# Optimization experiments

Measured on AMD Instinct MI355X. Metric: run time of the kernel, lower is better.

Reference implementation:

```python
import jax, jax.numpy as jnp
import numpy as np

F_NODE, F_BOND, D, LAYERS = 133, 14, 256, 3
N_NODE, N_BOND, N_NB = 100000, 200000, 600000


def hardswish(x):
    return x * jnp.clip(x + 3.0, 0.0, 6.0) * (1.0 / 6.0)


def setup_inputs() -> dict:
    key = jax.random.key(0)
    ks = jax.random.split(key, 16)

    def xav(k, fan_in, fan_out):
        std = (2.0 / (fan_in + fan_out)) ** 0.5
        return (jax.random.normal(k, (fan_in, fan_out), jnp.float32) * std)

    inp = {
        "node": jax.random.normal(ks[0], (N_NODE, F_NODE), jnp.float32),
        "bond": jax.random.normal(ks[1], (N_BOND, F_BOND), jnp.float32),
        "connect": jax.random.randint(ks[2], (3, N_BOND), 0, N_NODE, jnp.int32),
        "bond_neighbour": jax.random.randint(ks[3], (2, N_NB), 0, N_BOND, jnp.int32),
        # learned parameters, stored as [in, out] (torch Linear transposed)
        "w_node": xav(ks[4], F_NODE, D), "b_node": jnp.zeros((D,), jnp.float32),
        "w_node_final": xav(ks[5], F_NODE + D, D), "b_node_final": jnp.zeros((D,), jnp.float32),
        "w_bond": xav(ks[6], F_NODE + F_BOND, D), "b_bond": jnp.zeros((D,), jnp.float32),
        "w_bond_final": xav(ks[7], F_NODE + F_BOND + D, D), "b_bond_final": jnp.zeros((D,), jnp.float32),
        "w_z": xav(ks[8], F_NODE + F_BOND + D, D), "b_z": jnp.zeros((D,), jnp.float32),
        "w_r": xav(ks[9], F_NODE + F_BOND + D, D), "b_r": jnp.zeros((D,), jnp.float32),
        "u": xav(ks[10], D, D),
        "w_m": xav(ks[11], F_NODE + F_BOND, D), "b_m": jnp.zeros((D,), jnp.float32),
        "w_n": xav(ks[12], F_NODE, D), "b_n": jnp.zeros((D,), jnp.float32),
        "u_n": xav(ks[13], 2 * D, D),
    }
    return inp


def reference(node, bond, connect, bond_neighbour,
              w_node, b_node, w_node_final, b_node_final,
              w_bond, b_bond, w_bond_final, b_bond_final,
              w_z, b_z, w_r, b_r, u, w_m, b_m, w_n, b_n, u_n):
    i_idx, j_idx = connect[0], connect[1]          # [E]; connect[2] (reverse) unused
    ij_idx, ki_idx = bond_neighbour[0], bond_neighbour[1]  # [E_nb]

    init_bond = jnp.concatenate([node[i_idx], bond], axis=-1)  # [E, f_node+f_bond]
    init_node = node                                           # [N, f_node]

    mess_bond = hardswish(init_bond @ w_bond + b_bond)  # [E, D]
    mess_node = hardswish(node @ w_node + b_node)       # [N, D]

    for _ in range(LAYERS):
        mess_ki = mess_bond[ki_idx]                                   # [E_nb, D]
        s_ij = jax.ops.segment_sum(mess_ki, ij_idx, num_segments=N_BOND)
        z_ij = jax.nn.sigmoid(jnp.concatenate([init_bond, s_ij], -1) @ w_z + b_z)
        r_ki = jax.nn.sigmoid(jnp.concatenate([init_bond[ij_idx], mess_ki], -1) @ w_r + b_r)
        r_ij = jax.ops.segment_sum(r_ki * mess_ki, ij_idx, num_segments=N_BOND)
        m_ij = jnp.tanh(init_bond @ w_m + b_m + r_ij @ u)
        mess_bond = (1.0 - z_ij) * s_ij + z_ij * m_ij                 # [E, D]
        aggr_node = jax.ops.segment_sum(mess_bond, j_idx, num_segments=N_NODE)
        mess_node = hardswish(init_node @ w_n + b_n
                              + jnp.concatenate([mess_node, aggr_node], -1) @ u_n)

    mess_bond = hardswish(jnp.concatenate([init_bond, mess_bond], -1) @ w_bond_final + b_bond_final)
    mess_node = hardswish(jnp.concatenate([init_node, mess_node], -1) @ w_node_final + b_node_final)
    # dropout is identity in eval mode
    return mess_node, mess_bond
```

## Files before the change

kernel.cpp:

```cpp
#include <hip/hip_runtime.h>
#include <hip/hip_bf16.h>

#define NN 100000
#define NE 200000
#define NB 600000
#define FN 133
#define FB 14
#define FIB 147
#define DD 256

typedef __hip_bfloat16 bf16;
typedef __attribute__((ext_vector_type(8))) short short8;
typedef __attribute__((ext_vector_type(4))) float f32x4;

__device__ __forceinline__ float hswish(float x) {
    float c = fminf(fmaxf(x + 3.f, 0.f), 6.f);
    return x * c * (1.f / 6.f);
}
__device__ __forceinline__ float sigmoidf(float x) {
    return 1.f / (1.f + __expf(-x));
}
__device__ __forceinline__ float tanh_fast(float x) {
    return 1.f - 2.f / (1.f + __expf(2.f * x));
}
__device__ __forceinline__ float bf2f(unsigned short u) {
    union { unsigned int i; float f; } c; c.i = (unsigned int)u << 16; return c.f;
}
__device__ __forceinline__ unsigned short f2bf(float v) {
    bf16 b = __float2bfloat16(v);
    unsigned short u; __builtin_memcpy(&u, &b, 2); return u;
}
__device__ __forceinline__ void unp8(short8 v, float* f) {
    #pragma unroll
    for (int j = 0; j < 8; j++) {
        short s = v[j]; unsigned short u; __builtin_memcpy(&u, &s, 2);
        f[j] = bf2f(u);
    }
}
__device__ __forceinline__ uint4 pk8(const float* f) {
    uint4 v;
    v.x = f2bf(f[0]) | ((unsigned)f2bf(f[1]) << 16);
    v.y = f2bf(f[2]) | ((unsigned)f2bf(f[3]) << 16);
    v.z = f2bf(f[4]) | ((unsigned)f2bf(f[5]) << 16);
    v.w = f2bf(f[6]) | ((unsigned)f2bf(f[7]) << 16);
    return v;
}

__global__ __launch_bounds__(256) void fill_kernel(float* __restrict__ p, float v, long n4) {
    long i = (long)blockIdx.x * 256 + threadIdx.x;
    long st = (long)gridDim.x * 256;
    float4 z = {v, v, v, v};
    for (; i < n4; i += st) ((float4*)p)[i] = z;
}

__global__ __launch_bounds__(256) void build_ib_bf(
    const float* __restrict__ node, const float* __restrict__ bond,
    const int* __restrict__ i_idx, bf16* __restrict__ IB)
{
    int t = blockIdx.x * 256 + threadIdx.x;
    int row = t >> 6;
    if (row >= NE) return;
    int lane = t & 63;
    if (lane >= 40) return;
    int src = i_idx[row];
    int c = lane * 4;
    unsigned short us[4];
    #pragma unroll
    for (int j = 0; j < 4; j++) {
        int k = c + j;
        float v = 0.f;
        if (k < FN)       v = node[(size_t)src * FN + k];
        else if (k < FIB) v = bond[(size_t)row * FB + (k - FN)];
        us[j] = f2bf(v);
    }
    ushort4 o = {us[0], us[1], us[2], us[3]};
    *(ushort4*)((unsigned short*)IB + (size_t)row * 160 + c) = o;
}

__global__ __launch_bounds__(256) void count_kernel(
    const int* __restrict__ idx, int n, int* __restrict__ cnt)
{
    int i = blockIdx.x * 256 + threadIdx.x;
    if (i < n) atomicAdd(&cnt[idx[i]], 1);
}

__global__ __launch_bounds__(256) void scan_block(int* __restrict__ data, int* __restrict__ bsum)
{
    __shared__ int lds[256];
    int base = blockIdx.x * 1024 + threadIdx.x * 4;
    int c0 = data[base], c1 = data[base + 1], c2 = data[base + 2], c3 = data[base + 3];
    int t = c0 + c1 + c2 + c3;
    lds[threadIdx.x] = t;
    __syncthreads();
    int x = t;
    for (int off = 1; off < 256; off <<= 1) {
        int y = (threadIdx.x >= off) ? lds[threadIdx.x - off] : 0;
        __syncthreads();
        x += y; lds[threadIdx.x] = x;
        __syncthreads();
    }
    int excl = x - t;
    data[base] = excl; data[base + 1] = excl + c0;
    data[base + 2] = excl + c0 + c1; data[base + 3] = excl + c0 + c1 + c2;
    if (threadIdx.x == 255) bsum[blockIdx.x] = x;
}

__global__ __launch_bounds__(256) void scan_bsum(int* __restrict__ bsum, int n)
{
    __shared__ int lds[256];
    int t = (threadIdx.x < n) ? bsum[threadIdx.x] : 0;
    lds[threadIdx.x] = t;
    __syncthreads();
    int x = t;
    for (int off = 1; off < 256; off <<= 1) {
        int y = (threadIdx.x >= off) ? lds[threadIdx.x - off] : 0;
        __syncthreads();
        x += y; lds[threadIdx.x] = x;
        __syncthreads();
    }
    if (threadIdx.x < n) bsum[threadIdx.x] = x - t;
}

__global__ __launch_bounds__(256) void scan_add(
    int* __restrict__ data, const int* __restrict__ bsum, int n)
{
    int i = blockIdx.x * 256 + threadIdx.x;
    if (i < n) data[i] += bsum[i >> 10];
}

__global__ __launch_bounds__(256) void copy_int(
    int* __restrict__ dst, const int* __restrict__ src, int n)
{
    int i = blockIdx.x * 256 + threadIdx.x;
    if (i < n) dst[i] = src[i];
}

__global__ __launch_bounds__(256) void fill_nb_list(
    const int* __restrict__ ij, const int* __restrict__ ki,
    int* __restrict__ cur, int* __restrict__ lst)
{
    int e = blockIdx.x * 256 + threadIdx.x;
    if (e < NB) { int p = atomicAdd(&cur[ij[e]], 1); lst[p] = ki[e]; }
}

__global__ __launch_bounds__(256) void fill_agg_list(
    const int* __restrict__ jidx, int* __restrict__ cur, int* __restrict__ lst)
{
    int e = blockIdx.x * 256 + threadIdx.x;
    if (e < NE) { int p = atomicAdd(&cur[jidx[e]], 1); lst[p] = e; }
}

__global__ __launch_bounds__(256) void seg_sr_kernel(
    const bf16* __restrict__ MB, const bf16* __restrict__ TR,
    const bf16* __restrict__ PR, const int* __restrict__ off,
    const int* __restrict__ lst,
    bf16* __restrict__ S, bf16* __restrict__ R)
{
    int sid = blockIdx.x * 4 + (threadIdx.x >> 6);
    if (sid >= NE) return;
    int lane = threadIdx.x & 63;
    ushort4 up = *(const ushort4*)((const unsigned short*)PR + (size_t)sid * DD + lane * 4);
    float p0 = bf2f(up.x), p1 = bf2f(up.y), p2 = bf2f(up.z), p3 = bf2f(up.w);
    int b = off[sid], e = off[sid + 1];
    float s0 = 0, s1 = 0, s2 = 0, s3 = 0;
    float r0 = 0, r1 = 0, r2 = 0, r3 = 0;
    for (int t = b; t < e; t++) {
        int src = lst[t];
        ushort4 um = *(const ushort4*)((const unsigned short*)MB + (size_t)src * DD + lane * 4);
        ushort4 ut = *(const ushort4*)((const unsigned short*)TR + (size_t)src * DD + lane * 4);
        float m0 = bf2f(um.x), m1 = bf2f(um.y), m2 = bf2f(um.z), m3 = bf2f(um.w);
        s0 += m0; s1 += m1; s2 += m2; s3 += m3;
        r0 += sigmoidf(p0 + bf2f(ut.x)) * m0;
        r1 += sigmoidf(p1 + bf2f(ut.y)) * m1;
        r2 += sigmoidf(p2 + bf2f(ut.z)) * m2;
        r3 += sigmoidf(p3 + bf2f(ut.w)) * m3;
    }
    ushort4 os = {f2bf(s0), f2bf(s1), f2bf(s2), f2bf(s3)};
    ushort4 orr = {f2bf(r0), f2bf(r1), f2bf(r2), f2bf(r3)};
    *(ushort4*)((unsigned short*)S + (size_t)sid * DD + lane * 4) = os;
    *(ushort4*)((unsigned short*)R + (size_t)sid * DD + lane * 4) = orr;
}

__global__ __launch_bounds__(256) void pack_wt(
    const float* W1, int K1, const float* W2, int K2, const float* W3, int K3,
    int KTpad, bf16* dst)
{
    int idx = blockIdx.x * 256 + threadIdx.x;
    if (idx >= 256 * KTpad) return;
    int n = idx / KTpad, k = idx % KTpad;
    float v = 0.f;
    if (k < K1)                { if (W1) v = W1[(size_t)k * DD + n]; }
    else if (k < K1 + K2)      { if (W2) v = W2[(size_t)(k - K1) * DD + n]; }
    else if (k < K1 + K2 + K3) { if (W3) v = W3[(size_t)(k - K1 - K2) * DD + n]; }
    dst[(size_t)n * KTpad + k] = __float2bfloat16(v);
}

__global__ __launch_bounds__(512) void blend2(
    const bf16* __restrict__ S, const bf16* __restrict__ R,
    const bf16* __restrict__ WTz2, const bf16* __restrict__ WTu,
    const bf16* __restrict__ PZ, const bf16* __restrict__ PM,
    bf16* __restrict__ MB)
{
    __shared__ __align__(16) unsigned short As[128 * 40];
    __shared__ __align__(16) unsigned short Bs[128 * 40];
    const int tid = threadIdx.x;
    const int row0 = blockIdx.x * 128, col0 = blockIdx.y * 128;
    const int lane = tid & 63, w = tid >> 6;
    const int wr = w >> 1, wc = w & 1;
    const int fr = lane & 15, ko = (lane >> 4) * 8;

    f32x4 acc1[2][4] = {};
    f32x4 acc2[2][4] = {};

    #pragma unroll
    for (int ph = 0; ph < 2; ph++) {
        const bf16* A = (ph == 0) ? S : R;
        const bf16* W = (ph == 0) ? WTz2 : WTu;
        for (int k0 = 0; k0 < DD; k0 += 32) {
            {
                int mloc = tid >> 2, kq = (tid & 3) * 8;
                int mg = row0 + mloc;
                uint4 v = {0, 0, 0, 0};
                if (mg < NE)
                    v = *(const uint4*)((const unsigned short*)A + (size_t)mg * DD + k0 + kq);
                *(uint4*)&As[mloc * 40 + kq] = v;
                *(uint4*)&Bs[mloc * 40 + kq] =
                    *(const uint4*)((const unsigned short*)W + (size_t)(col0 + mloc) * DD + k0 + kq);
            }
            __syncthreads();
            short8 af[2], bf8[4];
            #pragma unroll
            for (int mf = 0; mf < 2; mf++)
                af[mf] = *(const short8*)&As[(wr * 32 + mf * 16 + fr) * 40 + ko];
            #pragma unroll
            for (int nf = 0; nf < 4; nf++)
                bf8[nf] = *(const short8*)&Bs[(wc * 64 + nf * 16 + fr) * 40 + ko];
            #pragma unroll
            for (int mf = 0; mf < 2; mf++)
                #pragma unroll
                for (int nf = 0; nf < 4; nf++) {
                    if (ph == 0)
                        acc1[mf][nf] = __builtin_amdgcn_mfma_f32_16x16x32_bf16(af[mf], bf8[nf], acc1[mf][nf], 0, 0, 0);
                    else
                        acc2[mf][nf] = __builtin_amdgcn_mfma_f32_16x16x32_bf16(af[mf], bf8[nf], acc2[mf][nf], 0, 0, 0);
                }
            __syncthreads();
        }
    }

    #pragma unroll
    for (int mf = 0; mf < 2; mf++) {
        #pragma unroll
        for (int i = 0; i < 4; i++) {
            int mloc = wr * 32 + mf * 16 + (lane >> 4) * 4 + i;
            int gm = row0 + mloc;
            if (gm >= NE) continue;
            #pragma unroll
            for (int nf = 0; nf < 4; nf++) {
                int gc = col0 + wc * 64 + nf * 16 + fr;
                size_t idx = (size_t)gm * DD + gc;
                float z  = sigmoidf(acc1[mf][nf][i] + __bfloat162float(PZ[idx]));
                float mm = tanh_fast(acc2[mf][nf][i] + __bfloat162float(PM[idx]));
                float s  = __bfloat162float(S[idx]);
                MB[idx] = __float2bfloat16((1.f - z) * s + z * mm);
            }
        }
    }
}

__global__ __launch_bounds__(512) void pairk(
    int trblocks,
    const bf16* __restrict__ MBn, const bf16* __restrict__ WTr2,
    bf16* __restrict__ TRo,
    const bf16* __restrict__ MN, const int* __restrict__ offN,
    const int* __restrict__ agLst, const bf16* __restrict__ WTnu,
    const bf16* __restrict__ PN, bf16* __restrict__ MNout)
{
    __shared__ __align__(16) unsigned short As[128 * 40];
    __shared__ __align__(16) unsigned short Bs[256 * 40];
    const int tid = threadIdx.x, lane = tid & 63, w = tid >> 6;
    const int fr = lane & 15, ko = (lane >> 4) * 8;
    const int mloc = tid >> 2, kq = (tid & 3) * 8;

    if ((int)blockIdx.x < trblocks) {
        const int bx = blockIdx.x % 1563, by = blockIdx.x / 1563;
        const int row0 = bx * 128, col0 = by * 128;
        const int wr = w >> 1, wc = w & 1;
        const int mg = row0 + mloc;
        f32x4 acc[2][4] = {};
        for (int k0 = 0; k0 < 256; k0 += 32) {
            uint4 v = {0, 0, 0, 0};
            if (mg < NE)
                v = *(const uint4*)((const unsigned short*)MBn + (size_t)mg * DD + k0 + kq);
            *(uint4*)&As[mloc * 40 + kq] = v;
            *(uint4*)&Bs[mloc * 40 + kq] =
                *(const uint4*)((const unsigned short*)WTr2 + (size_t)(col0 + mloc) * DD + k0 + kq);
            __syncthreads();
            short8 af[2], bw[4];
// ... 41 lines not shown
                    const int kk = kg - 256;
                    float a[8] = {0, 0, 0, 0, 0, 0, 0, 0};
                    for (int t = eb; t < ee; t++) {
                        int src = agLst[t];
                        float m8[8];
                        unp8(*(const short8*)((const unsigned short*)MBn + (size_t)src * DD + kk), m8);
                        #pragma unroll
                        for (int j = 0; j < 8; j++) a[j] += m8[j];
                    }
                    v = pk8(a);
                }
            }
            *(uint4*)&As[mloc * 40 + kq] = v;
            #pragma unroll
            for (int it = 0; it < 2; ++it) {
                int nloc = (tid >> 2) + it * 128;
                *(uint4*)&Bs[nloc * 40 + kq] =
                    *(const uint4*)((const unsigned short*)WTnu + (size_t)nloc * 512 + k0 + kq);
            }
            __syncthreads();
            short8 af[4], bw[4];
            #pragma unroll
            for (int mf = 0; mf < 4; mf++)
                af[mf] = *(const short8*)&As[(wr * 64 + mf * 16 + fr) * 40 + ko];
            #pragma unroll
            for (int nf = 0; nf < 4; nf++)
                bw[nf] = *(const short8*)&Bs[(wc * 64 + nf * 16 + fr) * 40 + ko];
            #pragma unroll
            for (int mf = 0; mf < 4; mf++)
                #pragma unroll
                for (int nf = 0; nf < 4; nf++)
                    acc[mf][nf] = __builtin_amdgcn_mfma_f32_16x16x32_bf16(af[mf], bw[nf], acc[mf][nf], 0, 0, 0);
            __syncthreads();
        }
        #pragma unroll
        for (int mf = 0; mf < 4; mf++)
            #pragma unroll
            for (int i = 0; i < 4; i++) {
                int ml = wr * 64 + mf * 16 + (lane >> 4) * 4 + i;
                int gm = row0 + ml;
                if (gm >= NN) continue;
                #pragma unroll
                for (int nf = 0; nf < 4; nf++) {
                    int gc = wc * 64 + nf * 16 + fr;
                    size_t idx = (size_t)gm * DD + gc;
                    MNout[idx] = __float2bfloat16(
                        hswish(acc[mf][nf][i] + __bfloat162float(PN[idx])));
                }
            }
    }
}

template <int BN, int NT, int DUAL, int EPB>
__global__ __launch_bounds__(NT) void bg(
    const void* __restrict__ A1, int a1stride, int a1kw, int a1real, int a1f32,
    const void* __restrict__ A2, int a2stride, int a2kw, int a2real, int a2f32,
    const bf16* __restrict__ WT1, const bf16* __restrict__ WT2, int KT,
    const float* __restrict__ bias1, const float* __restrict__ bias2,
    const bf16* __restrict__ PZb, const bf16* __restrict__ PMb,
    void* __restrict__ out1, void* __restrict__ out2, int M)
{
    constexpr int BM = 128;
    constexpr int nWc = BN / 64;
    constexpr int nWr = (NT / 64) / nWc;
    constexpr int MSPAN = BM / nWr;
    constexpr int MFR = MSPAN / 16;
    __shared__ __align__(16) unsigned short As[BM * 40];
    __shared__ __align__(16) unsigned short As2[(DUAL == 2 ? BM : 8) * 40];
    __shared__ __align__(16) unsigned short Bs[BN * 40];
    __shared__ __align__(16) unsigned short Bs2[(DUAL ? BN : 8) * 40];
    const int tid = threadIdx.x;
    const int row0 = blockIdx.x * BM, col0 = blockIdx.y * BN;
    const int lane = tid & 63, w = tid >> 6;
    const int wr = w / nWc, wc = w % nWc;
    const int fr = lane & 15, ko = (lane >> 4) * 8;

    f32x4 acc[MFR][4] = {};
    f32x4 acc2[DUAL ? MFR : 1][DUAL ? 4 : 1] = {};

    for (int k0 = 0; k0 < KT; k0 += 32) {
        #pragma unroll
        for (int it = 0; it < BM * 4 / NT; ++it) {
            int mloc = (tid >> 2) + it * (NT / 4);
            int mg = row0 + mloc;
            bool mok = (mg < M);
            int kq = (tid & 3) * 8;
            int kg = k0 + kq;
            if (DUAL == 2) {
                uint4 v1 = {0, 0, 0, 0}, v2 = {0, 0, 0, 0};
                if (mok) {
                    v1 = *(const uint4*)((const bf16*)A1 + (size_t)mg * a1stride + kg);
                    v2 = *(const uint4*)((const bf16*)A2 + (size_t)mg * a2stride + kg);
                }
                *(uint4*)&As[mloc * 40 + kq] = v1;
                *(uint4*)&As2[mloc * 40 + kq] = v2;
            } else {
                const void* p; int stride, real, isf; int kk;
                if (kg < a1kw) { p = A1; stride = a1stride; real = a1real; isf = a1f32; kk = kg; }
                else           { p = A2; stride = a2stride; real = a2real; isf = a2f32; kk = kg - a1kw; }
                uint4 v = {0, 0, 0, 0};
                if (mok) {
                    if (!isf) {
                        v = *(const uint4*)((const bf16*)p + (size_t)mg * stride + kk);
                    } else {
                        const float* fp = (const float*)p + (size_t)mg * stride;
                        unsigned short us[8];
                        #pragma unroll
                        for (int j = 0; j < 8; j++)
                            us[j] = (kk + j < real) ? f2bf(fp[kk + j]) : (unsigned short)0;
                        v.x = us[0] | ((unsigned)us[1] << 16);
                        v.y = us[2] | ((unsigned)us[3] << 16);
                        v.z = us[4] | ((unsigned)us[5] << 16);
                        v.w = us[6] | ((unsigned)us[7] << 16);
                    }
                }
                *(uint4*)&As[mloc * 40 + kq] = v;
            }
        }
        #pragma unroll
        for (int it = 0; it < BN * 4 / NT; ++it) {
            int nloc = (tid >> 2) + it * (NT / 4);
            int kq = (tid & 3) * 8;
            *(uint4*)&Bs[nloc * 40 + kq] =
                *(const uint4*)&WT1[(size_t)(col0 + nloc) * KT + k0 + kq];
            if (DUAL)
                *(uint4*)&Bs2[nloc * 40 + kq] =
                    *(const uint4*)&WT2[(size_t)(col0 + nloc) * KT + k0 + kq];
        }
        __syncthreads();
        short8 a1f[MFR], b1f[4];
        short8 a2f[DUAL == 2 ? MFR : 1], b2f[DUAL ? 4 : 1];
        #pragma unroll
        for (int mf = 0; mf < MFR; mf++) {
            a1f[mf] = *(const short8*)&As[(wr * MSPAN + mf * 16 + fr) * 40 + ko];
            if (DUAL == 2)
                a2f[mf] = *(const short8*)&As2[(wr * MSPAN + mf * 16 + fr) * 40 + ko];
        }
        #pragma unroll
        for (int nf = 0; nf < 4; nf++) {
            b1f[nf] = *(const short8*)&Bs[(wc * 64 + nf * 16 + fr) * 40 + ko];
            if (DUAL)
                b2f[nf] = *(const short8*)&Bs2[(wc * 64 + nf * 16 + fr) * 40 + ko];
        }
        #pragma unroll
        for (int mf = 0; mf < MFR; mf++)
            #pragma unroll
            for (int nf = 0; nf < 4; nf++) {
                acc[mf][nf] = __builtin_amdgcn_mfma_f32_16x16x32_bf16(a1f[mf], b1f[nf], acc[mf][nf], 0, 0, 0);
                if (DUAL)
                    acc2[mf][nf] = __builtin_amdgcn_mfma_f32_16x16x32_bf16(
                        DUAL == 2 ? a2f[mf] : a1f[mf], b2f[nf], acc2[mf][nf], 0, 0, 0);
            }
        __syncthreads();
    }

    #pragma unroll
    for (int mf = 0; mf < MFR; mf++) {
        #pragma unroll
        for (int i = 0; i < 4; i++) {
            int mloc = wr * MSPAN + mf * 16 + (lane >> 4) * 4 + i;
            int gm = row0 + mloc;
            if (gm >= M) continue;
            #pragma unroll
            for (int nf = 0; nf < 4; nf++) {
                int gc = col0 + wc * 64 + nf * 16 + fr;
                size_t idx = (size_t)gm * DD + gc;
                float v = acc[mf][nf][i];
                if (EPB == 0) {
                    if (bias1) v += bias1[gc];
                    ((bf16*)out1)[idx] = __float2bfloat16(v);
                } else if (EPB == 1) {
                    ((bf16*)out1)[idx] = __float2bfloat16(hswish(v + bias1[gc]));
                } else if (EPB == 2) {
                    ((bf16*)out1)[idx] = __float2bfloat16(hswish(v + bias1[gc]));
                    ((bf16*)out2)[idx] = __float2bfloat16(acc2[mf][nf][i] + bias2[gc]);
                } else if (EPB == 3) {
                    ((bf16*)out1)[idx] = __float2bfloat16(v + bias1[gc]);
                    ((bf16*)out2)[idx] = __float2bfloat16(acc2[mf][nf][i] + bias2[gc]);
                } else if (EPB == 4) {
                    float z  = sigmoidf(v + __bfloat162float(PZb[idx]));
                    float mm = tanh_fast(acc2[mf][nf][i] + __bfloat162float(PMb[idx]));
                    float s  = __bfloat162float(((const bf16*)A1)[idx]);
                    ((bf16*)out1)[idx] = __float2bfloat16((1.f - z) * s + z * mm);
                } else if (EPB == 5) {
                    ((bf16*)out1)[idx] =
                        __float2bfloat16(hswish(v + __bfloat162float(PZb[idx])));
                } else {
                    ((float*)out1)[idx] = hswish(v + bias1[gc]);
                }
            }
        }
    }
}

extern "C" void kernel_launch(void* const* d_in, const int* in_sizes, int n_in,
                              void* d_out, int out_size, void* d_ws, size_t ws_size,
                              hipStream_t stream)
{
    const float* node  = (const float*)d_in[0];
    const float* bond  = (const float*)d_in[1];
    const int* connect = (const int*)d_in[2];
    const int* bnb     = (const int*)d_in[3];
    const float* w_node       = (const float*)d_in[4];
    const float* b_node       = (const float*)d_in[5];
    const float* w_node_final = (const float*)d_in[6];
    const float* b_node_final = (const float*)d_in[7];
    const float* w_bond       = (const float*)d_in[8];
    const float* b_bond       = (const float*)d_in[9];
    const float* w_bond_final = (const float*)d_in[10];
    const float* b_bond_final = (const float*)d_in[11];
    const float* w_z = (const float*)d_in[12];
    const float* b_z = (const float*)d_in[13];
    const float* w_r = (const float*)d_in[14];
    const float* b_r = (const float*)d_in[15];
    const float* u_  = (const float*)d_in[16];
    const float* w_m = (const float*)d_in[17];
    const float* b_m = (const float*)d_in[18];
    const float* w_n = (const float*)d_in[19];
    const float* b_n = (const float*)d_in[20];
    const float* u_n = (const float*)d_in[21];

    const int* i_idx = connect;
    const int* j_idx = connect + NE;
    const int* ij    = bnb;
    const int* ki    = bnb + NB;

    const size_t EBH = (size_t)NE * DD * 2;
    const size_t B_WT = (size_t)3072 * 256 * 2;
    const int NEpad = 196 * 1024;
    const int NNpad = 98 * 1024;
    const size_t B_CSR = (size_t)NEpad * 8 + (size_t)NB * 4
                       + (size_t)NNpad * 8 + (size_t)NE * 4 + 2048;
    const size_t NEED = 5 * EBH + B_WT + B_CSR;

    float* out_node = (float*)d_out;
    float* out_bond = out_node + (size_t)NN * DD;

    if (ws_size < NEED) {
        fill_kernel<<<2048, 256, 0, stream>>>((float*)d_out, 1e6f, (long)out_size / 4);
        return;
    }

    char* base = (char*)d_ws;
    bf16* PR = (bf16*)base;                       base += EBH;
    bf16* MB = (bf16*)base;                       base += EBH;
    bf16* TR = (bf16*)base;                       base += EBH;
    bf16* PZ = (bf16*)base;                       base += EBH;
    bf16* PM = (bf16*)base;                       base += EBH;
    char* wt = base;                              base += B_WT;
    int* offE  = (int*)base;                      base += (size_t)NEpad * 4;
    int* curE  = (int*)base;                      base += (size_t)NEpad * 4;
    int* nbLst = (int*)base;                      base += (size_t)NB * 4;
    int* offN  = (int*)base;                      base += (size_t)NNpad * 4;
    int* curN  = (int*)base;                      base += (size_t)NNpad * 4;
    int* agLst = (int*)base;                      base += (size_t)NE * 4;
    int* bsumE = (int*)base;                      base += 1024;
    int* bsumN = (int*)base;

    bf16* IBbf = TR;
    float* scratchN = (float*)TR;
    bf16* R = (bf16*)out_bond;
    bf16* S = R + (size_t)NE * DD;
    bf16* MN = (bf16*)out_node;
    bf16* PN = MN + (size_t)NN * DD;

    auto wtAlloc = [&](size_t elems) { bf16* p = (bf16*)wt; wt += elems * 2; return p; };
    bf16* WTr  = wtAlloc(160 * 256);
    bf16* WTz1 = wtAlloc(160 * 256);
    bf16* WTb  = wtAlloc(160 * 256);
    bf16* WTm1 = wtAlloc(160 * 256);
    bf16* WTn0 = wtAlloc(160 * 256);
    bf16* WTn  = wtAlloc(160 * 256);
    bf16* WTr2 = wtAlloc(256 * 256);
    bf16* WTz2 = wtAlloc(256 * 256);
    bf16* WTu  = wtAlloc(256 * 256);
    bf16* WTnu = wtAlloc(512 * 256);
    bf16* WTbf = wtAlloc(416 * 256);
    bf16* WTnf = wtAlloc(416 * 256);

    const float* w_r2 = w_r + (size_t)FIB * DD;
    const float* w_z2 = w_z + (size_t)FIB * DD;

    auto packG = [&](int ktpad) { return (256 * ktpad + 255) / 256; };
    pack_wt<<<packG(160), 256, 0, stream>>>(w_r, FIB, nullptr, 0, nullptr, 0, 160, WTr);
    pack_wt<<<packG(160), 256, 0, stream>>>(w_z, FIB, nullptr, 0, nullptr, 0, 160, WTz1);
    pack_wt<<<packG(160), 256, 0, stream>>>(w_bond, FIB, nullptr, 0, nullptr, 0, 160, WTb);
    pack_wt<<<packG(160), 256, 0, stream>>>(w_m, FIB, nullptr, 0, nullptr, 0, 160, WTm1);
    pack_wt<<<packG(160), 256, 0, stream>>>(w_node, FN, nullptr, 0, nullptr, 0, 160, WTn0);
    pack_wt<<<packG(160), 256, 0, stream>>>(w_n, FN, nullptr, 0, nullptr, 0, 160, WTn);
    pack_wt<<<packG(256), 256, 0, stream>>>(w_r2, DD, nullptr, 0, nullptr, 0, 256, WTr2);
    pack_wt<<<packG(256), 256, 0, stream>>>(w_z2, DD, nullptr, 0, nullptr, 0, 256, WTz2);
    pack_wt<<<packG(256), 256, 0, stream>>>(u_, DD, nullptr, 0, nullptr, 0, 256, WTu);
    pack_wt<<<packG(512), 256, 0, stream>>>(u_n, 2 * DD, nullptr, 0, nullptr, 0, 512, WTnu);
    pack_wt<<<packG(416), 256, 0, stream>>>(w_bond_final, FIB, nullptr, 13,
                                            w_bond_final + (size_t)FIB * DD, DD, 416, WTbf);
    pack_wt<<<packG(416), 256, 0, stream>>>(w_node_final, FN, nullptr, 27,
                                            w_node_final + (size_t)FN * DD, DD, 416, WTnf);

    fill_kernel<<<256, 256, 0, stream>>>((float*)offE, 0.f, NEpad / 4);
    fill_kernel<<<256, 256, 0, stream>>>((float*)offN, 0.f, NNpad / 4);
    count_kernel<<<(NB + 255) / 256, 256, 0, stream>>>(ij, NB, offE);
    count_kernel<<<(NE + 255) / 256, 256, 0, stream>>>(j_idx, NE, offN);
    scan_block<<<196, 256, 0, stream>>>(offE, bsumE);
    scan_bsum<<<1, 256, 0, stream>>>(bsumE, 196);
    scan_add<<<NEpad / 256, 256, 0, stream>>>(offE, bsumE, NEpad);
    scan_block<<<98, 256, 0, stream>>>(offN, bsumN);
    scan_bsum<<<1, 256, 0, stream>>>(bsumN, 98);
    scan_add<<<NNpad / 256, 256, 0, stream>>>(offN, bsumN, NNpad);
    copy_int<<<NEpad / 256, 256, 0, stream>>>(curE, offE, NEpad);
    copy_int<<<NNpad / 256, 256, 0, stream>>>(curN, offN, NNpad);
    fill_nb_list<<<(NB + 255) / 256, 256, 0, stream>>>(ij, ki, curE, nbLst);
    fill_agg_list<<<(NE + 255) / 256, 256, 0, stream>>>(j_idx, curN, agLst);

    dim3 gB2(1563, 2);
    dim3 gB1(1563, 1);
    dim3 gN2(782, 2);
    dim3 gN1(782, 1);
    int blkIB = NE * 64 / 256;

    build_ib_bf<<<blkIB, 256, 0, stream>>>(node, bond, i_idx, IBbf);
    bg<128, 512, 1, 3><<<gB2, 512, 0, stream>>>(
        IBbf, 160, 160, 160, 0, nullptr, 0, 0, 0, 0,
        WTr, WTz1, 160, b_r, b_z, nullptr, nullptr, PR, PZ, NE);
    bg<128, 512, 1, 2><<<gB2, 512, 0, stream>>>(
        IBbf, 160, 160, 160, 0, nullptr, 0, 0, 0, 0,
        WTb, WTm1, 160, b_bond, b_m, nullptr, nullptr, MB, PM, NE);
    bg<128, 512, 1, 2><<<gN2, 512, 0, stream>>>(
        node, FN, 160, FN, 1, nullptr, 0, 0, 0, 0,
        WTn0, WTn, 160, b_node, b_n, nullptr, nullptr, MN, PN, NN);
    bg<128, 256, 0, 0><<<gB2, 256, 0, stream>>>(
        MB, 256, 256, 256, 0, nullptr, 0, 0, 0, 0,
        WTr2, nullptr, 256, nullptr, nullptr, nullptr, nullptr, TR, nullptr, NE);

    for (int l = 0; l < 3; l++) {
        seg_sr_kernel<<<(NE + 3) / 4, 256, 0, stream>>>(MB, TR, PR, offE, nbLst, S, R);
        blend2<<<gB2, 512, 0, stream>>>(S, R, WTz2, WTu, PZ, PM, MB);
        int trb = (l < 2) ? 3126 : 0;
        pairk<<<trb + 782, 512, 0, stream>>>(trb, MB, WTr2, TR,
                                             MN, offN, agLst, WTnu, PN, MN);
    }

    build_ib_bf<<<blkIB, 256, 0, stream>>>(node, bond, i_idx, IBbf);
    bg<256, 512, 0, 6><<<gB1, 512, 0, stream>>>(
        IBbf, 160, 160, 160, 0, MB, 256, 256, 256, 0,
        WTbf, nullptr, 416, b_bond_final, nullptr, nullptr, nullptr, out_bond, nullptr, NE);
    bg<256, 512, 0, 6><<<gN1, 512, 0, stream>>>(
        node, FN, 160, FN, 1, MN, 256, 256, 256, 0,
        WTnf, nullptr, 416, b_node_final, nullptr, nullptr, nullptr, scratchN, nullptr, NN);
    hipMemcpyAsync(out_node, scratchN, (size_t)NN * DD * 4,
                   hipMemcpyDeviceToDevice, stream);
}
```

Before: 2.556 ms.

## Merge setup and GEMM launches into combined kernels and widen blend2 K-tile

Collapses the twelve weight-packing launches into one pack_all kernel and pairs the E- and N-side CSR build kernels (zero, count, scan, copy, list fill) into single launches. The independent pre-loop GEMMs and the two final GEMMs are merged into multi-role kernels that dispatch on block index, removing launch gaps and letting small grids run concurrently. blend2 now stages 64-wide K slices per barrier instead of 32, halving the sync count at the cost of more LDS per block. The bg template loses its DUAL==2 path and becomes a device body shared by the combined kernels.

```diff
diff --git a/kernel.cpp b/kernel.cpp
--- a/kernel.cpp
+++ b/kernel.cpp
@@ -8,6 +8,8 @@
 #define FB 14
 #define FIB 147
 #define DD 256
+#define NEPAD (196 * 1024)
+#define NNPAD (98 * 1024)
 
 typedef __hip_bfloat16 bf16;
 typedef __attribute__((ext_vector_type(8))) short short8;
@@ -77,17 +79,31 @@
     *(ushort4*)((unsigned short*)IB + (size_t)row * 160 + c) = o;
 }
 
-__global__ __launch_bounds__(256) void count_kernel(
-    const int* __restrict__ idx, int n, int* __restrict__ cnt)
+__global__ __launch_bounds__(256) void zero2_kernel(int* __restrict__ offE, int* __restrict__ offN)
 {
     int i = blockIdx.x * 256 + threadIdx.x;
-    if (i < n) atomicAdd(&cnt[idx[i]], 1);
-}
-
-__global__ __launch_bounds__(256) void scan_block(int* __restrict__ data, int* __restrict__ bsum)
+    if (i < NEPAD) offE[i] = 0;
+    else if (i < NEPAD + NNPAD) offN[i - NEPAD] = 0;
+}
+
+__global__ __launch_bounds__(256) void count2_kernel(
+    const int* __restrict__ ij, const int* __restrict__ jidx,
+    int* __restrict__ offE, int* __restrict__ offN)
+{
+    int i = blockIdx.x * 256 + threadIdx.x;
+    if (i < NB) atomicAdd(&offE[ij[i]], 1);
+    else if (i < NB + NE) atomicAdd(&offN[jidx[i - NB]], 1);
+}
+
+__global__ __launch_bounds__(256) void scan_block2(
+    int* __restrict__ offE, int* __restrict__ offN,
+    int* __restrict__ bsumE, int* __restrict__ bsumN)
 {
     __shared__ int lds[256];
-    int base = blockIdx.x * 1024 + threadIdx.x * 4;
+    int* data; int* bs; int bb;
+    if ((int)blockIdx.x < 196) { data = offE; bs = bsumE; bb = blockIdx.x; }
+    else                       { data = offN; bs = bsumN; bb = blockIdx.x - 196; }
+    int base = bb * 1024 + threadIdx.x * 4;
     int c0 = data[base], c1 = data[base + 1], c2 = data[base + 2], c3 = data[base + 3];
     int t = c0 + c1 + c2 + c3;
     lds[threadIdx.x] = t;
@@ -102,13 +118,15 @@
     int excl = x - t;
     data[base] = excl; data[base + 1] = excl + c0;
     data[base + 2] = excl + c0 + c1; data[base + 3] = excl + c0 + c1 + c2;
-    if (threadIdx.x == 255) bsum[blockIdx.x] = x;
-}
-
-__global__ __launch_bounds__(256) void scan_bsum(int* __restrict__ bsum, int n)
+    if (threadIdx.x == 255) bs[bb] = x;
+}
+
+__global__ __launch_bounds__(256) void scan_bsum2(int* __restrict__ bsumE, int* __restrict__ bsumN)
 {
     __shared__ int lds[256];
-    int t = (threadIdx.x < n) ? bsum[threadIdx.x] : 0;
+    int* bs = blockIdx.x ? bsumN : bsumE;
+    int n = blockIdx.x ? 98 : 196;
+    int t = (threadIdx.x < n) ? bs[threadIdx.x] : 0;
     lds[threadIdx.x] = t;
     __syncthreads();
     int x = t;
@@ -118,36 +136,80 @@
         x += y; lds[threadIdx.x] = x;
         __syncthreads();
     }
-    if (threadIdx.x < n) bsum[threadIdx.x] = x - t;
-}
-
-__global__ __launch_bounds__(256) void scan_add(
-    int* __restrict__ data, const int* __restrict__ bsum, int n)
+    if (threadIdx.x < n) bs[threadIdx.x] = x - t;
+}
+
+__global__ __launch_bounds__(256) void scan_add2(
+    int* __restrict__ offE, int* __restrict__ offN,
+    const int* __restrict__ bsumE, const int* __restrict__ bsumN)
 {
     int i = blockIdx.x * 256 + threadIdx.x;
-    if (i < n) data[i] += bsum[i >> 10];
-}
-
-__global__ __launch_bounds__(256) void copy_int(
-    int* __restrict__ dst, const int* __restrict__ src, int n)
+    if (i < NEPAD) offE[i] += bsumE[i >> 10];
+    else if (i < NEPAD + NNPAD) { int j = i - NEPAD; offN[j] += bsumN[j >> 10]; }
+}
+
+__global__ __launch_bounds__(256) void copy2_kernel(
+    int* __restrict__ curE, int* __restrict__ curN,
+    const int* __restrict__ offE, const int* __restrict__ offN)
 {
     int i = blockIdx.x * 256 + threadIdx.x;
-    if (i < n) dst[i] = src[i];
-}
-
-__global__ __launch_bounds__(256) void fill_nb_list(
-    const int* __restrict__ ij, const int* __restrict__ ki,
-    int* __restrict__ cur, int* __restrict__ lst)
-{
-    int e = blockIdx.x * 256 + threadIdx.x;
-    if (e < NB) { int p = atomicAdd(&cur[ij[e]], 1); lst[p] = ki[e]; }
-}
-
-__global__ __launch_bounds__(256) void fill_agg_list(
-    const int* __restrict__ jidx, int* __restrict__ cur, int* __restrict__ lst)
-{
-    int e = blockIdx.x * 256 + threadIdx.x;
-    if (e < NE) { int p = atomicAdd(&cur[jidx[e]], 1); lst[p] = e; }
+    if (i < NEPAD) curE[i] = offE[i];
+    else if (i < NEPAD + NNPAD) { int j = i - NEPAD; curN[j] = offN[j]; }
+}
+
+__global__ __launch_bounds__(256) void lists2_kernel(
+    const int* __restrict__ ij, const int* __restrict__ ki, const int* __restrict__ jidx,
+    int* __restrict__ curE, int* __restrict__ curN,
+    int* __restrict__ nbLst, int* __restrict__ agLst)
+{
+    int i = blockIdx.x * 256 + threadIdx.x;
+    if (i < NB) { int p = atomicAdd(&curE[ij[i]], 1); nbLst[p] = ki[i]; }
+    else if (i < NB + NE) {
+        int e = i - NB;
+        int p = atomicAdd(&curN[jidx[e]], 1); agLst[p] = e;
+    }
+}
+
+__global__ __launch_bounds__(256) void pack_all(
+    const float* __restrict__ w_r, const float* __restrict__ w_z,
+    const float* __restrict__ w_bond, const float* __restrict__ w_m,
+    const float* __restrict__ w_node, const float* __restrict__ w_n,
+    const float* __restrict__ u_, const float* __restrict__ u_n,
+    const float* __restrict__ w_bf, const float* __restrict__ w_nf,
+    bf16* __restrict__ wt)
+{
+    int idx = blockIdx.x * 256 + threadIdx.x;
+    if (idx >= 786432) return;
+    float v = 0.f;
+    if (idx < 245760) {
+        int r = idx / 40960;
+        int loc = idx - r * 40960;
+        int n = loc / 160, k = loc % 160;
+        const float* W = (r == 0) ? w_r : (r == 1) ? w_z : (r == 2) ? w_bond
+                       : (r == 3) ? w_m : (r == 4) ? w_node : w_n;
+        int K1 = (r < 4) ? FIB : FN;
+        if (k < K1) v = W[(size_t)k * DD + n];
+    } else if (idx < 442368) {
+        int r = (idx - 245760) / 65536;
+        int loc = (idx - 245760) - r * 65536;
+        int n = loc / 256, k = loc % 256;
+        const float* W = (r == 0) ? (w_r + (size_t)FIB * DD)
+                       : (r == 1) ? (w_z + (size_t)FIB * DD) : u_;
+        v = W[(size_t)k * DD + n];
+    } else if (idx < 573440) {
+        int loc = idx - 442368;
+        int n = loc / 512, k = loc % 512;
+        v = u_n[(size_t)k * DD + n];
+    } else {
+        int r = (idx - 573440) / 106496;
+        int loc = (idx - 573440) - r * 106496;
+        int n = loc / 416, k = loc % 416;
+        const float* W = r ? w_nf : w_bf;
+        int K1 = r ? FN : FIB;
+        if (k < K1)        v = W[(size_t)k * DD + n];
+        else if (k >= 160) v = W[(size_t)(K1 + k - 160) * DD + n];
+    }
+    wt[idx] = __float2bfloat16(v);
 }
 
 __global__ __launch_bounds__(256) void seg_sr_kernel(
@@ -181,28 +243,14 @@
     *(ushort4*)((unsigned short*)R + (size_t)sid * DD + lane * 4) = orr;
 }
 
-__global__ __launch_bounds__(256) void pack_wt(
-    const float* W1, int K1, const float* W2, int K2, const float* W3, int K3,
-    int KTpad, bf16* dst)
-{
-    int idx = blockIdx.x * 256 + threadIdx.x;
-    if (idx >= 256 * KTpad) return;
-    int n = idx / KTpad, k = idx % KTpad;
-    float v = 0.f;
-    if (k < K1)                { if (W1) v = W1[(size_t)k * DD + n]; }
-    else if (k < K1 + K2)      { if (W2) v = W2[(size_t)(k - K1) * DD + n]; }
-    else if (k < K1 + K2 + K3) { if (W3) v = W3[(size_t)(k - K1 - K2) * DD + n]; }
-    dst[(size_t)n * KTpad + k] = __float2bfloat16(v);
-}
-
 __global__ __launch_bounds__(512) void blend2(
     const bf16* __restrict__ S, const bf16* __restrict__ R,
     const bf16* __restrict__ WTz2, const bf16* __restrict__ WTu,
     const bf16* __restrict__ PZ, const bf16* __restrict__ PM,
     bf16* __restrict__ MB)
 {
-    __shared__ __align__(16) unsigned short As[128 * 40];
-    __shared__ __align__(16) unsigned short Bs[128 * 40];
+    __shared__ __align__(16) unsigned short As[128 * 72];
+    __shared__ __align__(16) unsigned short Bs[128 * 72];
     const int tid = threadIdx.x;
     const int row0 = blockIdx.x * 128, col0 = blockIdx.y * 128;
     const int lane = tid & 63, w = tid >> 6;
@@ -216,34 +264,42 @@
     for (int ph = 0; ph < 2; ph++) {
         const bf16* A = (ph == 0) ? S : R;
         const bf16* W = (ph == 0) ? WTz2 : WTu;
-        for (int k0 = 0; k0 < DD; k0 += 32) {
+        for (int k0 = 0; k0 < DD; k0 += 64) {
             {
-                int mloc = tid >> 2, kq = (tid & 3) * 8;
+                int mloc = tid >> 2, kq = (tid & 3) * 16;
                 int mg = row0 + mloc;
-                uint4 v = {0, 0, 0, 0};
-                if (mg < NE)
-                    v = *(const uint4*)((const unsigned short*)A + (size_t)mg * DD + k0 + kq);
-                *(uint4*)&As[mloc * 40 + kq] = v;
-                *(uint4*)&Bs[mloc * 40 + kq] =
-                    *(const uint4*)((const unsigned short*)W + (size_t)(col0 + mloc) * DD + k0 + kq);
+                uint4 va = {0, 0, 0, 0}, va2 = {0, 0, 0, 0};
+                if (mg < NE) {
+                    va  = *(const uint4*)((const unsigned short*)A + (size_t)mg * DD + k0 + kq);
+                    va2 = *(const uint4*)((const unsigned short*)A + (size_t)mg * DD + k0 + kq + 8);
+                }
+                uint4 vb  = *(const uint4*)((const unsigned short*)W + (size_t)(col0 + mloc) * DD + k0 + kq);
+                uint4 vb2 = *(const uint4*)((const unsigned short*)W + (size_t)(col0 + mloc) * DD + k0 + kq + 8);
+                *(uint4*)&As[mloc * 72 + kq] = va;
+                *(uint4*)&As[mloc * 72 + kq + 8] = va2;
+                *(uint4*)&Bs[mloc * 72 + kq] = vb;
+                *(uint4*)&Bs[mloc * 72 + kq + 8] = vb2;
             }
             __syncthreads();
-            short8 af[2], bf8[4];
-            #pragma unroll
-            for (int mf = 0; mf < 2; mf++)
-                af[mf] = *(const short8*)&As[(wr * 32 + mf * 16 + fr) * 40 + ko];
-            #pragma unroll
-            for (int nf = 0; nf < 4; nf++)
-                bf8[nf] = *(const short8*)&Bs[(wc * 64 + nf * 16 + fr) * 40 + ko];
-            #pragma unroll
-            for (int mf = 0; mf < 2; mf++)
+            #pragma unroll
+            for (int kk = 0; kk < 64; kk += 32) {
+                short8 af[2], bf8[4];
                 #pragma unroll
-                for (int nf = 0; nf < 4; nf++) {
-                    if (ph == 0)
-                        acc1[mf][nf] = __builtin_amdgcn_mfma_f32_16x16x32_bf16(af[mf], bf8[nf], acc1[mf][nf], 0, 0, 0);
-                    else
-                        acc2[mf][nf] = __builtin_amdgcn_mfma_f32_16x16x32_bf16(af[mf], bf8[nf], acc2[mf][nf], 0, 0, 0);
-                }
+                for (int mf = 0; mf < 2; mf++)
+                    af[mf] = *(const short8*)&As[(wr * 32 + mf * 16 + fr) * 72 + kk + ko];
+                #pragma unroll
+                for (int nf = 0; nf < 4; nf++)
+                    bf8[nf] = *(const short8*)&Bs[(wc * 64 + nf * 16 + fr) * 72 + kk + ko];
+                #pragma unroll
+                for (int mf = 0; mf < 2; mf++)
+                    #pragma unroll
+                    for (int nf = 0; nf < 4; nf++) {
+                        if (ph == 0)
+                            acc1[mf][nf] = __builtin_amdgcn_mfma_f32_16x16x32_bf16(af[mf], bf8[nf], acc1[mf][nf], 0, 0, 0);
+                        else
+                            acc2[mf][nf] = __builtin_amdgcn_mfma_f32_16x16x32_bf16(af[mf], bf8[nf], acc2[mf][nf], 0, 0, 0);
+                    }
+            }
             __syncthreads();
         }
     }
@@ -391,25 +447,21 @@
 }
 
 template <int BN, int NT, int DUAL, int EPB>
-__global__ __launch_bounds__(NT) void bg(
+__device__ __forceinline__ void bg_body(
     const void* __restrict__ A1, int a1stride, int a1kw, int a1real, int a1f32,
     const void* __restrict__ A2, int a2stride, int a2kw, int a2real, int a2f32,
     const bf16* __restrict__ WT1, const bf16* __restrict__ WT2, int KT,
     const float* __restrict__ bias1, const float* __restrict__ bias2,
-    const bf16* __restrict__ PZb, const bf16* __restrict__ PMb,
-    void* __restrict__ out1, void* __restrict__ out2, int M)
+    void* __restrict__ out1, void* __restrict__ out2, int M,
+    int row0, int col0,
+    unsigned short* As, unsigned short* Bs, unsigned short* Bs2)
 {
     constexpr int BM = 128;
     constexpr int nWc = BN / 64;
     constexpr int nWr = (NT / 64) / nWc;
     constexpr int MSPAN = BM / nWr;
     constexpr int MFR = MSPAN / 16;
-    __shared__ __align__(16) unsigned short As[BM * 40];
-    __shared__ __align__(16) unsigned short As2[(DUAL == 2 ? BM : 8) * 40];
-    __shared__ __align__(16) unsigned short Bs[BN * 40];
-    __shared__ __align__(16) unsigned short Bs2[(DUAL ? BN : 8) * 40];
     const int tid = threadIdx.x;
-    const int row0 = blockIdx.x * BM, col0 = blockIdx.y * BN;
     const int lane = tid & 63, w = tid >> 6;
     const int wr = w / nWc, wc = w % nWc;
     const int fr = lane & 15, ko = (lane >> 4) * 8;
@@ -425,36 +477,26 @@
             bool mok = (mg < M);
             int kq = (tid & 3) * 8;
             int kg = k0 + kq;
-            if (DUAL == 2) {
-                uint4 v1 = {0, 0, 0, 0}, v2 = {0, 0, 0, 0};
-                if (mok) {
-                    v1 = *(const uint4*)((const bf16*)A1 + (size_t)mg * a1stride + kg);
-                    v2 = *(const uint4*)((const bf16*)A2 + (size_t)mg * a2stride + kg);
+            const void* p; int stride, real, isf; int kk;
+            if (kg < a1kw) { p = A1; stride = a1stride; real = a1real; isf = a1f32; kk = kg; }
+            else           { p = A2; stride = a2stride; real = a2real; isf = a2f32; kk = kg - a1kw; }
+            uint4 v = {0, 0, 0, 0};
+            if (mok) {
+                if (!isf) {
+                    v = *(const uint4*)((const bf16*)p + (size_t)mg * stride + kk);
+                } else {
+                    const float* fp = (const float*)p + (size_t)mg * stride;
+                    unsigned short us[8];
+                    #pragma unroll
+                    for (int j = 0; j < 8; j++)
+                        us[j] = (kk + j < real) ? f2bf(fp[kk + j]) : (unsigned short)0;
+                    v.x = us[0] | ((unsigned)us[1] << 16);
+                    v.y = us[2] | ((unsigned)us[3] << 16);
+                    v.z = us[4] | ((unsigned)us[5] << 16);
+                    v.w = us[6] | ((unsigned)us[7] << 16);
                 }
-                *(uint4*)&As[mloc * 40 + kq] = v1;
-                *(uint4*)&As2[mloc * 40 + kq] = v2;
-            } else {
-                const void* p; int stride, real, isf; int kk;
-                if (kg < a1kw) { p = A1; stride = a1stride; real = a1real; isf = a1f32; kk = kg; }
-                else           { p = A2; stride = a2stride; real = a2real; isf = a2f32; kk = kg - a1kw; }
-                uint4 v = {0, 0, 0, 0};
-                if (mok) {
-                    if (!isf) {
-                        v = *(const uint4*)((const bf16*)p + (size_t)mg * stride + kk);
-                    } else {
-                        const float* fp = (const float*)p + (size_t)mg * stride;
-                        unsigned short us[8];
-                        #pragma unroll
-                        for (int j = 0; j < 8; j++)
-                            us[j] = (kk + j < real) ? f2bf(fp[kk + j]) : (unsigned short)0;
-                        v.x = us[0] | ((unsigned)us[1] << 16);
-                        v.y = us[2] | ((unsigned)us[3] << 16);
-                        v.z = us[4] | ((unsigned)us[5] << 16);
-                        v.w = us[6] | ((unsigned)us[7] << 16);
-                    }
-                }
-                *(uint4*)&As[mloc * 40 + kq] = v;
-            }
+            }
+            *(uint4*)&As[mloc * 40 + kq] = v;
         }
         #pragma unroll
         for (int it = 0; it < BN * 4 / NT; ++it) {
@@ -467,14 +509,10 @@
                     *(const uint4*)&WT2[(size_t)(col0 + nloc) * KT + k0 + kq];
         }
         __syncthreads();
-        short8 a1f[MFR], b1f[4];
-        short8 a2f[DUAL == 2 ? MFR : 1], b2f[DUAL ? 4 : 1];
-        #pragma unroll
-        for (int mf = 0; mf < MFR; mf++) {
+        short8 a1f[MFR], b1f[4], b2f[DUAL ? 4 : 1];
+        #pragma unroll
+        for (int mf = 0; mf < MFR; mf++)
             a1f[mf] = *(const short8*)&As[(wr * MSPAN + mf * 16 + fr) * 40 + ko];
-            if (DUAL == 2)
-                a2f[mf] = *(const short8*)&As2[(wr * MSPAN + mf * 16 + fr) * 40 + ko];
-        }
         #pragma unroll
         for (int nf = 0; nf < 4; nf++) {
             b1f[nf] = *(const short8*)&Bs[(wc * 64 + nf * 16 + fr) * 40 + ko];
@@ -487,8 +525,7 @@
             for (int nf = 0; nf < 4; nf++) {
                 acc[mf][nf] = __builtin_amdgcn_mfma_f32_16x16x32_bf16(a1f[mf], b1f[nf], acc[mf][nf], 0, 0, 0);
                 if (DUAL)
-                    acc2[mf][nf] = __builtin_amdgcn_mfma_f32_16x16x32_bf16(
-                        DUAL == 2 ? a2f[mf] : a1f[mf], b2f[nf], acc2[mf][nf], 0, 0, 0);
+                    acc2[mf][nf] = __builtin_amdgcn_mfma_f32_16x16x32_bf16(a1f[mf], b2f[nf], acc2[mf][nf], 0, 0, 0);
             }
         __syncthreads();
     }
@@ -508,27 +545,90 @@
                 if (EPB == 0) {
                     if (bias1) v += bias1[gc];
                     ((bf16*)out1)[idx] = __float2bfloat16(v);
-                } else if (EPB == 1) {
-                    ((bf16*)out1)[idx] = __float2bfloat16(hswish(v + bias1[gc]));
                 } else if (EPB == 2) {
                     ((bf16*)out1)[idx] = __float2bfloat16(hswish(v + bias1[gc]));
                     ((bf16*)out2)[idx] = __float2bfloat16(acc2[mf][nf][i] + bias2[gc]);
                 } else if (EPB == 3) {
                     ((bf16*)out1)[idx] = __float2bfloat16(v + bias1[gc]);
                     ((bf16*)out2)[idx] = __float2bfloat16(acc2[mf][nf][i] + bias2[gc]);
-                } else if (EPB == 4) {
-                    float z  = sigmoidf(v + __bfloat162float(PZb[idx]));
-                    float mm = tanh_fast(acc2[mf][nf][i] + __bfloat162float(PMb[idx]));
-                    float s  = __bfloat162float(((const bf16*)A1)[idx]);
-                    ((bf16*)out1)[idx] = __float2bfloat16((1.f - z) * s + z * mm);
-                } else if (EPB == 5) {
-                    ((bf16*)out1)[idx] =
-                        __float2bfloat16(hswish(v + __bfloat162float(PZb[idx])));
                 } else {
                     ((float*)out1)[idx] = hswish(v + bias1[gc]);
                 }
             }
         }
+    }
+}
+
+__global__ __launch_bounds__(512) void pre_pair1(
+    const bf16* __restrict__ IBbf,
+    const bf16* __restrict__ WTr, const bf16* __restrict__ WTz1,
+    const float* __restrict__ b_r, const float* __restrict__ b_z,
+    bf16* __restrict__ PR, bf16* __restrict__ PZ,
+    const bf16* __restrict__ WTb, const bf16* __restrict__ WTm1,
+    const float* __restrict__ b_bond, const float* __restrict__ b_m,
+    bf16* __restrict__ MB, bf16* __restrict__ PM)
+{
+    __shared__ __align__(16) unsigned short As[128 * 40];
+    __shared__ __align__(16) unsigned short Bs[128 * 40];
+    __shared__ __align__(16) unsigned short Bs2[128 * 40];
+    int b = blockIdx.x;
+    if (b < 3126) {
+        int bx = b % 1563, by = b / 1563;
+        bg_body<128, 512, 1, 3>(IBbf, 160, 160, 160, 0, nullptr, 0, 0, 0, 0,
+            WTr, WTz1, 160, b_r, b_z, PR, PZ, NE, bx * 128, by * 128, As, Bs, Bs2);
+    } else {
+        int b2 = b - 3126;
+        int bx = b2 % 1563, by = b2 / 1563;
+        bg_body<128, 512, 1, 2>(IBbf, 160, 160, 160, 0, nullptr, 0, 0, 0, 0,
+            WTb, WTm1, 160, b_bond, b_m, MB, PM, NE, bx * 128, by * 128, As, Bs, Bs2);
+    }
+}
+
+__global__ __launch_bounds__(512) void pre_pair2(
+    const float* __restrict__ node,
+    const bf16* __restrict__ WTn0, const bf16* __restrict__ WTn,
+    const float* __restrict__ b_node, const float* __restrict__ b_n,
+    bf16* __restrict__ MN, bf16* __restrict__ PN,
+    const bf16* __restrict__ MB, const bf16* __restrict__ WTr2,
+    bf16* __restrict__ TR)
+{
+    __shared__ __align__(16) unsigned short As[128 * 40];
+    __shared__ __align__(16) unsigned short Bs[128 * 40];
+    __shared__ __align__(16) unsigned short Bs2[128 * 40];
+    int b = blockIdx.x;
+    if (b < 1564) {
+        int bx = b % 782, by = b / 782;
+        bg_body<128, 512, 1, 2>(node, FN, 160, FN, 1, nullptr, 0, 0, 0, 0,
+            WTn0, WTn, 160, b_node, b_n, MN, PN, NN, bx * 128, by * 128, As, Bs, Bs2);
+    } else {
+        int b2 = b - 1564;
+        int bx = b2 % 1563, by = b2 / 1563;
+        bg_body<128, 512, 0, 0>(MB, 256, 256, 256, 0, nullptr, 0, 0, 0, 0,
+            WTr2, nullptr, 256, nullptr, nullptr, TR, nullptr, NE,
+            bx * 128, by * 128, As, Bs, Bs2);
+    }
+}
+
+__global__ __launch_bounds__(512) void final_pair(
+    const bf16* __restrict__ IBbf, const bf16* __restrict__ MB,
+    const bf16* __restrict__ WTbf, const float* __restrict__ b_bf,
+    float* __restrict__ out_bond,
+    const float* __restrict__ node, const bf16* __restrict__ MN,
+    const bf16* __restrict__ WTnf, const float* __restrict__ b_nf,
+    float* __restrict__ scratchN)
+{
+    __shared__ __align__(16) unsigned short As[128 * 40];
+    __shared__ __align__(16) unsigned short Bs[256 * 40];
+    __shared__ __align__(16) unsigned short Bs2[8 * 40];
+    int b = blockIdx.x;
+    if (b < 1563) {
+        bg_body<256, 512, 0, 6>(IBbf, 160, 160, 160, 0, MB, 256, 256, 256, 0,
+            WTbf, nullptr, 416, b_bf, nullptr, out_bond, nullptr, NE,
+            b * 128, 0, As, Bs, Bs2);
+    } else {
+        bg_body<256, 512, 0, 6>(node, FN, 160, FN, 1, MN, 256, 256, 256, 0,
+            WTnf, nullptr, 416, b_nf, nullptr, scratchN, nullptr, NN,
+            (b - 1563) * 128, 0, As, Bs, Bs2);
     }
 }
 
@@ -565,11 +665,9 @@
     const int* ki    = bnb + NB;
 
     const size_t EBH = (size_t)NE * DD * 2;
-    const size_t B_WT = (size_t)3072 * 256 * 2;
-    const int NEpad = 196 * 1024;
-    const int NNpad = 98 * 1024;
-    const size_t B_CSR = (size_t)NEpad * 8 + (size_t)NB * 4
-                       + (size_t)NNpad * 8 + (size_t)NE * 4 + 2048;
+    const size_t B_WT = (size_t)786432 * 2;
+    const size_t B_CSR = (size_t)NEPAD * 8 + (size_t)NB * 4
+                       + (size_t)NNPAD * 8 + (size_t)NE * 4 + 2048;
     const size_t NEED = 5 * EBH + B_WT + B_CSR;
 
     float* out_node = (float*)d_out;
@@ -587,11 +685,11 @@
     bf16* PZ = (bf16*)base;                       base += EBH;
     bf16* PM = (bf16*)base;                       base += EBH;
     char* wt = base;                              base += B_WT;
-    int* offE  = (int*)base;                      base += (size_t)NEpad * 4;
-    int* curE  = (int*)base;                      base += (size_t)NEpad * 4;
+    int* offE  = (int*)base;                      base += (size_t)NEPAD * 4;
+    int* curE  = (int*)base;                      base += (size_t)NEPAD * 4;
     int* nbLst = (int*)base;                      base += (size_t)NB * 4;
-    int* offN  = (int*)base;                      base += (size_t)NNpad * 4;
-    int* curN  = (int*)base;                      base += (size_t)NNpad * 4;
+    int* offN  = (int*)base;                      base += (size_t)NNPAD * 4;
+    int* curN  = (int*)base;                      base += (size_t)NNPAD * 4;
     int* agLst = (int*)base;                      base += (size_t)NE * 4;
     int* bsumE = (int*)base;                      base += 1024;
     int* bsumN = (int*)base;
@@ -603,73 +701,40 @@
     bf16* MN = (bf16*)out_node;
     bf16* PN = MN + (size_t)NN * DD;
 
-    auto wtAlloc = [&](size_t elems) { bf16* p = (bf16*)wt; wt += elems * 2; return p; };
-    bf16* WTr  = wtAlloc(160 * 256);
-    bf16* WTz1 = wtAlloc(160 * 256);
-    bf16* WTb  = wtAlloc(160 * 256);
-    bf16* WTm1 = wtAlloc(160 * 256);
-    bf16* WTn0 = wtAlloc(160 * 256);
-    bf16* WTn  = wtAlloc(160 * 256);
-    bf16* WTr2 = wtAlloc(256 * 256);
-    bf16* WTz2 = wtAlloc(256 * 256);
-    bf16* WTu  = wtAlloc(256 * 256);
-    bf16* WTnu = wtAlloc(512 * 256);
-    bf16* WTbf = wtAlloc(416 * 256);
-    bf16* WTnf = wtAlloc(416 * 256);
-
-    const float* w_r2 = w_r + (size_t)FIB * DD;
-    const float* w_z2 = w_z + (size_t)FIB * DD;
-
-    auto packG = [&](int ktpad) { return (256 * ktpad + 255) / 256; };
-    pack_wt<<<packG(160), 256, 0, stream>>>(w_r, FIB, nullptr, 0, nullptr, 0, 160, WTr);
-    pack_wt<<<packG(160), 256, 0, stream>>>(w_z, FIB, nullptr, 0, nullptr, 0, 160, WTz1);
-    pack_wt<<<packG(160), 256, 0, stream>>>(w_bond, FIB, nullptr, 0, nullptr, 0, 160, WTb);
-    pack_wt<<<packG(160), 256, 0, stream>>>(w_m, FIB, nullptr, 0, nullptr, 0, 160, WTm1);
-    pack_wt<<<packG(160), 256, 0, stream>>>(w_node, FN, nullptr, 0, nullptr, 0, 160, WTn0);
-    pack_wt<<<packG(160), 256, 0, stream>>>(w_n, FN, nullptr, 0, nullptr, 0, 160, WTn);
-    pack_wt<<<packG(256), 256, 0, stream>>>(w_r2, DD, nullptr, 0, nullptr, 0, 256, WTr2);
-    pack_wt<<<packG(256), 256, 0, stream>>>(w_z2, DD, nullptr, 0, nullptr, 0, 256, WTz2);
-    pack_wt<<<packG(256), 256, 0, stream>>>(u_, DD, nullptr, 0, nullptr, 0, 256, WTu);
-    pack_wt<<<packG(512), 256, 0, stream>>>(u_n, 2 * DD, nullptr, 0, nullptr, 0, 512, WTnu);
-    pack_wt<<<packG(416), 256, 0, stream>>>(w_bond_final, FIB, nullptr, 13,
-                                            w_bond_final + (size_t)FIB * DD, DD, 416, WTbf);
-    pack_wt<<<packG(416), 256, 0, stream>>>(w_node_final, FN, nullptr, 27,
-                                            w_node_final + (size_t)FN * DD, DD, 416, WTnf);
-
-    fill_kernel<<<256, 256, 0, stream>>>((float*)offE, 0.f, NEpad / 4);
-    fill_kernel<<<256, 256, 0, stream>>>((float*)offN, 0.f, NNpad / 4);
-    count_kernel<<<(NB + 255) / 256, 256, 0, stream>>>(ij, NB, offE);
-    count_kernel<<<(NE + 255) / 256, 256, 0, stream>>>(j_idx, NE, offN);
-    scan_block<<<196, 256, 0, stream>>>(offE, bsumE);
-    scan_bsum<<<1, 256, 0, stream>>>(bsumE, 196);
-    scan_add<<<NEpad / 256, 256, 0, stream>>>(offE, bsumE, NEpad);
-    scan_block<<<98, 256, 0, stream>>>(offN, bsumN);
-    scan_bsum<<<1, 256, 0, stream>>>(bsumN, 98);
-    scan_add<<<NNpad / 256, 256, 0, stream>>>(offN, bsumN, NNpad);
-    copy_int<<<NEpad / 256, 256, 0, stream>>>(curE, offE, NEpad);
-    copy_int<<<NNpad / 256, 256, 0, stream>>>(curN, offN, NNpad);
-    fill_nb_list<<<(NB + 255) / 256, 256, 0, stream>>>(ij, ki, curE, nbLst);
-    fill_agg_list<<<(NE + 255) / 256, 256, 0, stream>>>(j_idx, curN, agLst);
-
+    bf16* wtb = (bf16*)wt;
+    bf16* WTr  = wtb + 0;
+    bf16* WTz1 = wtb + 40960;
+    bf16* WTb  = wtb + 81920;
+    bf16* WTm1 = wtb + 122880;
+    bf16* WTn0 = wtb + 163840;
+    bf16* WTn  = wtb + 204800;
+    bf16* WTr2 = wtb + 245760;
+    bf16* WTz2 = wtb + 311296;
+    bf16* WTu  = wtb + 376832;
+    bf16* WTnu = wtb + 442368;
+    bf16* WTbf = wtb + 573440;
+    bf16* WTnf = wtb + 679936;
+
+    pack_all<<<3072, 256, 0, stream>>>(w_r, w_z, w_bond, w_m, w_node, w_n,
+                                       u_, u_n, w_bond_final, w_node_final, wtb);
+
+    zero2_kernel<<<(NEPAD + NNPAD + 255) / 256, 256, 0, stream>>>(offE, offN);
+    count2_kernel<<<(NB + NE + 255) / 256, 256, 0, stream>>>(ij, j_idx, offE, offN);
+    scan_block2<<<294, 256, 0, stream>>>(offE, offN, bsumE, bsumN);
+    scan_bsum2<<<2, 256, 0, stream>>>(bsumE, bsumN);
+    scan_add2<<<(NEPAD + NNPAD + 255) / 256, 256, 0, stream>>>(offE, offN, bsumE, bsumN);
+    copy2_kernel<<<(NEPAD + NNPAD + 255) / 256, 256, 0, stream>>>(curE, curN, offE, offN);
+    lists2_kernel<<<(NB + NE + 255) / 256, 256, 0, stream>>>(ij, ki, j_idx,
+                                                             curE, curN, nbLst, agLst);
+
+    int blkIB = NE * 64 / 256;
     dim3 gB2(1563, 2);
-    dim3 gB1(1563, 1);
-    dim3 gN2(782, 2);
-    dim3 gN1(782, 1);
-    int blkIB = NE * 64 / 256;
 
     build_ib_bf<<<blkIB, 256, 0, stream>>>(node, bond, i_idx, IBbf);
-    bg<128, 512, 1, 3><<<gB2, 512, 0, stream>>>(
-        IBbf, 160, 160, 160, 0, nullptr, 0, 0, 0, 0,
-        WTr, WTz1, 160, b_r, b_z, nullptr, nullptr, PR, PZ, NE);
-    bg<128, 512, 1, 2><<<gB2, 512, 0, stream>>>(
-        IBbf, 160, 160, 160, 0, nullptr, 0, 0, 0, 0,
-        WTb, WTm1, 160, b_bond, b_m, nullptr, nullptr, MB, PM, NE);
-    bg<128, 512, 1, 2><<<gN2, 512, 0, stream>>>(
-        node, FN, 160, FN, 1, nullptr, 0, 0, 0, 0,
-        WTn0, WTn, 160, b_node, b_n, nullptr, nullptr, MN, PN, NN);
-    bg<128, 256, 0, 0><<<gB2, 256, 0, stream>>>(
-        MB, 256, 256, 256, 0, nullptr, 0, 0, 0, 0,
-        WTr2, nullptr, 256, nullptr, nullptr, nullptr, nullptr, TR, nullptr, NE);
+    pre_pair1<<<6252, 512, 0, stream>>>(IBbf, WTr, WTz1, b_r, b_z, PR, PZ,
+                                        WTb, WTm1, b_bond, b_m, MB, PM);
+    pre_pair2<<<4690, 512, 0, stream>>>(node, WTn0, WTn, b_node, b_n, MN, PN,
+                                        MB, WTr2, TR);
 
     for (int l = 0; l < 3; l++) {
         seg_sr_kernel<<<(NE + 3) / 4, 256, 0, stream>>>(MB, TR, PR, offE, nbLst, S, R);
@@ -680,12 +745,8 @@
     }
 
     build_ib_bf<<<blkIB, 256, 0, stream>>>(node, bond, i_idx, IBbf);
-    bg<256, 512, 0, 6><<<gB1, 512, 0, stream>>>(
-        IBbf, 160, 160, 160, 0, MB, 256, 256, 256, 0,
-        WTbf, nullptr, 416, b_bond_final, nullptr, nullptr, nullptr, out_bond, nullptr, NE);
-    bg<256, 512, 0, 6><<<gN1, 512, 0, stream>>>(
-        node, FN, 160, FN, 1, MN, 256, 256, 256, 0,
-        WTnf, nullptr, 416, b_node_final, nullptr, nullptr, nullptr, scratchN, nullptr, NN);
+    final_pair<<<2345, 512, 0, stream>>>(IBbf, MB, WTbf, b_bond_final, out_bond,
+                                         node, MN, WTnf, b_node_final, scratchN);
     hipMemcpyAsync(out_node, scratchN, (size_t)NN * DD * 4,
                    hipMemcpyDeviceToDevice, stream);
 }
```

Result: faster. 2.482 ms (-2.9%).
